# Kernel tuning notes

Hardware: AMD Instinct MI355X
Metric: run time of the kernel (lower is better)

## Reference

```python
import jax, jax.numpy as jnp
import numpy as np

B, N, D, C = 256, 256, 512, 1024
EPS = 1e-12  # F.normalize eps


def _l2norm(x):
    n = jnp.linalg.norm(x, axis=-1, keepdims=True)
    return x / jnp.maximum(n, EPS)


def setup_inputs() -> dict:
    key = jax.random.key(0)
    k1, k2, k3 = jax.random.split(key, 3)
    return {
        "image_tokens": jax.random.normal(k1, (B, N, D), dtype=jnp.float32),
        "text_features": jax.random.normal(k2, (C, D), dtype=jnp.float32),
        "log_tau": jnp.asarray(np.log(0.07), dtype=jnp.float32),
        "log_attn_tau": jnp.asarray(np.log(0.07), dtype=jnp.float32),
        "pid_labels": jax.random.randint(k3, (B,), 0, C),
    }


def reference(image_tokens, text_features, log_tau, log_attn_tau, pid_labels):
    toks = _l2norm(image_tokens.astype(jnp.float32))        # [B,N,D]
    txt = _l2norm(text_features.astype(jnp.float32))        # [C,D]
    sims = jnp.einsum('bnd,cd->bnc', toks, txt)             # [B,N,C]
    gt = pid_labels.astype(jnp.int32)
    # sims[arange(B), :, gt] -> [B,N]
    sims_gt = jnp.take_along_axis(sims, gt[:, None, None], axis=2)[..., 0]
    attn_tau = jnp.clip(jnp.exp(log_attn_tau), 0.01, 1.0)
    w = jax.nn.softmax(sims_gt / attn_tau, axis=1)          # [B,N]
    logits = jnp.einsum('bn,bnc->bc', w, sims)              # [B,C]
    tau = jnp.clip(jnp.exp(log_tau), 0.01, 1.0)
    logits = logits / tau
    # cross_entropy with label_smoothing=0.0, mean reduction
    logp = jax.nn.log_softmax(logits, axis=-1)
    nll = -jnp.take_along_axis(logp, gt[:, None], axis=1)[:, 0]
    return jnp.mean(nll)
```

## Files before the change

kernel.cpp:

```cpp
#include <hip/hip_runtime.h>
#include <math.h>

#define Bb 256
#define Nn 256
#define Dd 512
#define Cc 1024
#define KC 8
#define KD (Dd / KC)

__device__ __forceinline__ float waveReduceSum(float v) {
    #pragma unroll
    for (int off = 32; off > 0; off >>= 1)
        v += __shfl_xor(v, off, 64);
    return v;
}
__device__ __forceinline__ float waveReduceMax(float v) {
    #pragma unroll
    for (int off = 32; off > 0; off >>= 1)
        v = fmaxf(v, __shfl_xor(v, off, 64));
    return v;
}

__global__ void k_txtnorm(const float* __restrict__ txt, float* __restrict__ txt_n) {
    const int c = blockIdx.x;
    const int lane = threadIdx.x;
    const float* row = txt + (size_t)c * Dd + lane * 8;
    float4 a = *(const float4*)row;
    float4 b = *(const float4*)(row + 4);
    float ss = a.x*a.x + a.y*a.y + a.z*a.z + a.w*a.w
             + b.x*b.x + b.y*b.y + b.z*b.z + b.w*b.w;
    ss = waveReduceSum(ss);
    const float inv = 1.0f / fmaxf(sqrtf(ss), 1e-12f);
    float* out = txt_n + (size_t)c * Dd + lane * 8;
    a.x *= inv; a.y *= inv; a.z *= inv; a.w *= inv;
    b.x *= inv; b.y *= inv; b.z *= inv; b.w *= inv;
    *(float4*)out = a;
    *(float4*)(out + 4) = b;
}

__global__ void k_transpose(const float* __restrict__ txt_n, float* __restrict__ txt_t) {
    __shared__ float tile[32][33];
    const int c0 = blockIdx.x * 32;
    const int d0 = blockIdx.y * 32;
    const int tx = threadIdx.x & 31;
    const int ty = threadIdx.x >> 5;
    #pragma unroll
    for (int r = ty; r < 32; r += 8)
        tile[r][tx] = txt_n[(size_t)(c0 + r) * Dd + d0 + tx];
    __syncthreads();
    #pragma unroll
    for (int r = ty; r < 32; r += 8)
        txt_t[(size_t)(d0 + r) * Cc + c0 + tx] = tile[tx][r];
}

__global__ void __launch_bounds__(1024) k_attn_q(const float* __restrict__ toks,
                                                 const float* __restrict__ txt_n,
                                                 const int* __restrict__ pid,
                                                 const float* __restrict__ log_attn_tau,
                                                 float* __restrict__ q) {
    const int b = blockIdx.x;
    const int tid = threadIdx.x;
    const int wv = tid >> 6;
    const int lane = tid & 63;
    __shared__ float xg[Dd];
    __shared__ float qpart_s[16][Dd];
    __shared__ float ms[16], Ss[16];
    const int g = pid[b];
    if (tid < Dd) xg[tid] = txt_n[(size_t)g * Dd + tid];
    __syncthreads();
    float at = expf(log_attn_tau[0]);
    at = fminf(fmaxf(at, 0.01f), 1.0f);
    const float iat = 1.0f / at;

    const float4 xg0 = *(const float4*)&xg[lane * 8];
    const float4 xg1 = *(const float4*)&xg[lane * 8 + 4];

    float m = -INFINITY, S = 0.0f;
    float qa[8] = {0.f, 0.f, 0.f, 0.f, 0.f, 0.f, 0.f, 0.f};

    const float* base = toks + ((size_t)b * Nn + wv * 16) * Dd + lane * 8;
    float4 t0 = *(const float4*)base;
    float4 t1 = *(const float4*)(base + 4);
    #pragma unroll 4
    for (int r = 0; r < 16; ++r) {
        float4 n0, n1;
        if (r < 15) {
            const float* p = base + (size_t)(r + 1) * Dd;
            n0 = *(const float4*)p;
            n1 = *(const float4*)(p + 4);
        }
        float dot = t0.x*xg0.x + t0.y*xg0.y + t0.z*xg0.z + t0.w*xg0.w
                  + t1.x*xg1.x + t1.y*xg1.y + t1.z*xg1.z + t1.w*xg1.w;
        float ss  = t0.x*t0.x + t0.y*t0.y + t0.z*t0.z + t0.w*t0.w
                  + t1.x*t1.x + t1.y*t1.y + t1.z*t1.z + t1.w*t1.w;
        dot = waveReduceSum(dot);
        ss = waveReduceSum(ss);
        const float inv = 1.0f / fmaxf(sqrtf(ss), 1e-12f);
        const float s = dot * inv;
        if (s > m) {
            const float sc = expf((m - s) * iat);
            S = S * sc + 1.0f;
            qa[0] = qa[0]*sc + inv*t0.x; qa[1] = qa[1]*sc + inv*t0.y;
            qa[2] = qa[2]*sc + inv*t0.z; qa[3] = qa[3]*sc + inv*t0.w;
            qa[4] = qa[4]*sc + inv*t1.x; qa[5] = qa[5]*sc + inv*t1.y;
            qa[6] = qa[6]*sc + inv*t1.z; qa[7] = qa[7]*sc + inv*t1.w;
            m = s;
        } else {
            const float e = expf((s - m) * iat);
            S += e;
            const float w = e * inv;
            qa[0] = fmaf(w, t0.x, qa[0]); qa[1] = fmaf(w, t0.y, qa[1]);
            qa[2] = fmaf(w, t0.z, qa[2]); qa[3] = fmaf(w, t0.w, qa[3]);
            qa[4] = fmaf(w, t1.x, qa[4]); qa[5] = fmaf(w, t1.y, qa[5]);
            qa[6] = fmaf(w, t1.z, qa[6]); qa[7] = fmaf(w, t1.w, qa[7]);
        }
        t0 = n0; t1 = n1;
    }
    #pragma unroll
    for (int j = 0; j < 8; ++j) qpart_s[wv][lane * 8 + j] = qa[j];
    if (lane == 0) { ms[wv] = m; Ss[wv] = S; }
    __syncthreads();
    if (tid < Dd) {
        float M = -INFINITY;
        #pragma unroll
        for (int w = 0; w < 16; ++w) M = fmaxf(M, ms[w]);
        float Stot = 0.f, acc = 0.f;
        #pragma unroll
        for (int w = 0; w < 16; ++w) {
            const float sc = expf((ms[w] - M) * iat);
            Stot = fmaf(Ss[w], sc, Stot);
            acc = fmaf(qpart_s[w][tid], sc, acc);
        }
        q[(size_t)b * Dd + tid] = acc / Stot;
    }
}

__global__ void k_logits(const float* __restrict__ q, const float* __restrict__ txt_t,
                         float* __restrict__ part) {
    const int b0 = blockIdx.x * 4;
    const int kc = blockIdx.y;
    const int d0 = kc * KD;
    const int t = threadIdx.x;
    __shared__ float qs[4][KD];
    {
        const int j = t >> 6, d = t & 63;
        qs[j][d] = q[(size_t)(b0 + j) * Dd + d0 + d];
    }
    __syncthreads();
    const float4* xt = (const float4*)txt_t;
    float4 a0 = {0,0,0,0}, a1 = {0,0,0,0}, a2 = {0,0,0,0}, a3 = {0,0,0,0};
    #pragma unroll 4
    for (int d = 0; d < KD; d += 4) {
        const float4 q0 = *(const float4*)&qs[0][d];
        const float4 q1 = *(const float4*)&qs[1][d];
        const float4 q2 = *(const float4*)&qs[2][d];
        const float4 q3 = *(const float4*)&qs[3][d];
        const float4 x0 = xt[(size_t)(d0 + d + 0) * (Cc / 4) + t];
        const float4 x1 = xt[(size_t)(d0 + d + 1) * (Cc / 4) + t];
        const float4 x2 = xt[(size_t)(d0 + d + 2) * (Cc / 4) + t];
        const float4 x3 = xt[(size_t)(d0 + d + 3) * (Cc / 4) + t];
        a0.x = fmaf(q0.x,x0.x,a0.x); a0.y = fmaf(q0.x,x0.y,a0.y); a0.z = fmaf(q0.x,x0.z,a0.z); a0.w = fmaf(q0.x,x0.w,a0.w);
        a0.x = fmaf(q0.y,x1.x,a0.x); a0.y = fmaf(q0.y,x1.y,a0.y); a0.z = fmaf(q0.y,x1.z,a0.z); a0.w = fmaf(q0.y,x1.w,a0.w);
        a0.x = fmaf(q0.z,x2.x,a0.x); a0.y = fmaf(q0.z,x2.y,a0.y); a0.z = fmaf(q0.z,x2.z,a0.z); a0.w = fmaf(q0.z,x2.w,a0.w);
        a0.x = fmaf(q0.w,x3.x,a0.x); a0.y = fmaf(q0.w,x3.y,a0.y); a0.z = fmaf(q0.w,x3.z,a0.z); a0.w = fmaf(q0.w,x3.w,a0.w);
        a1.x = fmaf(q1.x,x0.x,a1.x); a1.y = fmaf(q1.x,x0.y,a1.y); a1.z = fmaf(q1.x,x0.z,a1.z); a1.w = fmaf(q1.x,x0.w,a1.w);
        a1.x = fmaf(q1.y,x1.x,a1.x); a1.y = fmaf(q1.y,x1.y,a1.y); a1.z = fmaf(q1.y,x1.z,a1.z); a1.w = fmaf(q1.y,x1.w,a1.w);
        a1.x = fmaf(q1.z,x2.x,a1.x); a1.y = fmaf(q1.z,x2.y,a1.y); a1.z = fmaf(q1.z,x2.z,a1.z); a1.w = fmaf(q1.z,x2.w,a1.w);
        a1.x = fmaf(q1.w,x3.x,a1.x); a1.y = fmaf(q1.w,x3.y,a1.y); a1.z = fmaf(q1.w,x3.z,a1.z); a1.w = fmaf(q1.w,x3.w,a1.w);
        a2.x = fmaf(q2.x,x0.x,a2.x); a2.y = fmaf(q2.x,x0.y,a2.y); a2.z = fmaf(q2.x,x0.z,a2.z); a2.w = fmaf(q2.x,x0.w,a2.w);
        a2.x = fmaf(q2.y,x1.x,a2.x); a2.y = fmaf(q2.y,x1.y,a2.y); a2.z = fmaf(q2.y,x1.z,a2.z); a2.w = fmaf(q2.y,x1.w,a2.w);
        a2.x = fmaf(q2.z,x2.x,a2.x); a2.y = fmaf(q2.z,x2.y,a2.y); a2.z = fmaf(q2.z,x2.z,a2.z); a2.w = fmaf(q2.z,x2.w,a2.w);
        a2.x = fmaf(q2.w,x3.x,a2.x); a2.y = fmaf(q2.w,x3.y,a2.y); a2.z = fmaf(q2.w,x3.z,a2.z); a2.w = fmaf(q2.w,x3.w,a2.w);
        a3.x = fmaf(q3.x,x0.x,a3.x); a3.y = fmaf(q3.x,x0.y,a3.y); a3.z = fmaf(q3.x,x0.z,a3.z); a3.w = fmaf(q3.x,x0.w,a3.w);
        a3.x = fmaf(q3.y,x1.x,a3.x); a3.y = fmaf(q3.y,x1.y,a3.y); a3.z = fmaf(q3.y,x1.z,a3.z); a3.w = fmaf(q3.y,x1.w,a3.w);
        a3.x = fmaf(q3.z,x2.x,a3.x); a3.y = fmaf(q3.z,x2.y,a3.y); a3.z = fmaf(q3.z,x2.z,a3.z); a3.w = fmaf(q3.z,x2.w,a3.w);
        a3.x = fmaf(q3.w,x3.x,a3.x); a3.y = fmaf(q3.w,x3.y,a3.y); a3.z = fmaf(q3.w,x3.z,a3.z); a3.w = fmaf(q3.w,x3.w,a3.w);
    }
    float* pb = part + ((size_t)kc * Bb + b0) * Cc;
    ((float4*)(pb + 0 * Cc))[t] = a0;
    ((float4*)(pb + 1 * Cc))[t] = a1;
    ((float4*)(pb + 2 * Cc))[t] = a2;
    ((float4*)(pb + 3 * Cc))[t] = a3;
}

__global__ void k_lse(const float* __restrict__ part, const int* __restrict__ pid,
                      const float* __restrict__ log_tau, float* __restrict__ nll) {
    const int b = blockIdx.x;
    const int t = threadIdx.x;
    float4 l = {0,0,0,0};
    #pragma unroll
    for (int kc = 0; kc < KC; ++kc) {
        const float4 p = ((const float4*)(part + ((size_t)kc * Bb + b) * Cc))[t];
        l.x += p.x; l.y += p.y; l.z += p.z; l.w += p.w;
    }
    float tau = expf(log_tau[0]);
    tau = fminf(fmaxf(tau, 0.01f), 1.0f);
    const float itau = 1.0f / tau;
    l.x *= itau; l.y *= itau; l.z *= itau; l.w *= itau;

    const int g = pid[b];
    __shared__ float redm[4], reds[4], sgt;
    if ((g >> 2) == t) {
        const float v[4] = {l.x, l.y, l.z, l.w};
        sgt = v[g & 3];
    }
    float m = fmaxf(fmaxf(l.x, l.y), fmaxf(l.z, l.w));
    m = waveReduceMax(m);
    if ((t & 63) == 0) redm[t >> 6] = m;
    __syncthreads();
    m = fmaxf(fmaxf(redm[0], redm[1]), fmaxf(redm[2], redm[3]));
    float e = expf(l.x - m) + expf(l.y - m) + expf(l.z - m) + expf(l.w - m);
    e = waveReduceSum(e);
    if ((t & 63) == 0) reds[t >> 6] = e;
    __syncthreads();
    if (t == 0) {
        const float S = reds[0] + reds[1] + reds[2] + reds[3];
        nll[b] = m + logf(S) - sgt;
    }
}

__global__ void k_mean(const float* __restrict__ nll, float* __restrict__ out) {
    float v = nll[threadIdx.x];
    __shared__ float red[4];
    v = waveReduceSum(v);
    if ((threadIdx.x & 63) == 0) red[threadIdx.x >> 6] = v;
    __syncthreads();
    if (threadIdx.x == 0) out[0] = (red[0] + red[1] + red[2] + red[3]) * (1.0f / (float)Bb);
}

extern "C" void kernel_launch(void* const* d_in, const int* in_sizes, int n_in,
                              void* d_out, int out_size, void* d_ws, size_t ws_size,
                              hipStream_t stream) {
    const float* toks = (const float*)d_in[0];
    const float* txt = (const float*)d_in[1];
    const float* log_tau = (const float*)d_in[2];
    const float* log_attn_tau = (const float*)d_in[3];
    const int* pid = (const int*)d_in[4];
    float* out = (float*)d_out;

    float* ws = (float*)d_ws;
    float* txt_n = ws;
    float* txt_t = txt_n + (size_t)Cc * Dd;
    float* q     = txt_t + (size_t)Dd * Cc;
    float* part  = q + (size_t)Bb * Dd;
    float* nll   = part + (size_t)KC * Bb * Cc;

    k_txtnorm<<<Cc, 64, 0, stream>>>(txt, txt_n);
    k_transpose<<<dim3(Cc / 32, Dd / 32), 256, 0, stream>>>(txt_n, txt_t);
    k_attn_q<<<Bb, 1024, 0, stream>>>(toks, txt_n, pid, log_attn_tau, q);
    k_logits<<<dim3(Bb / 4, KC), 256, 0, stream>>>(q, txt_t, part);
    k_lse<<<Bb, 256, 0, stream>>>(part, pid, log_tau, nll);
    k_mean<<<1, 256, 0, stream>>>(nll, out);
}
```

Before: 219.1 us.

## Fuse text normalization with transpose and fold mean into LSE via atomics

Merges the text-normalization and transpose kernels into one prep kernel that loads 16 rows into padded shared memory, computes per-row inverse norms, and writes the normalized transposed matrix directly. The separate normalized copy is dropped, and attention reads raw text scaled by the stored inverse norm. The final mean kernel is removed: each LSE block atomically adds its scaled NLL into an output zeroed by a memset. This cuts launches and one full pass over the text matrix, at the cost of nondeterministic float summation order and a memset call.

Measured after the change: 222.6 us. No clear change (+1.6%).

```diff
diff --git a/kernel.cpp b/kernel.cpp
--- a/kernel.cpp
+++ b/kernel.cpp
@@ -7,6 +7,8 @@
 #define Cc 1024
 #define KC 8
 #define KD (Dd / KC)
+#define PR 16
+#define PSTR 516
 
 __device__ __forceinline__ float waveReduceSum(float v) {
     #pragma unroll
@@ -21,40 +23,51 @@
     return v;
 }
 
-__global__ void k_txtnorm(const float* __restrict__ txt, float* __restrict__ txt_n) {
-    const int c = blockIdx.x;
-    const int lane = threadIdx.x;
-    const float* row = txt + (size_t)c * Dd + lane * 8;
-    float4 a = *(const float4*)row;
-    float4 b = *(const float4*)(row + 4);
-    float ss = a.x*a.x + a.y*a.y + a.z*a.z + a.w*a.w
-             + b.x*b.x + b.y*b.y + b.z*b.z + b.w*b.w;
-    ss = waveReduceSum(ss);
-    const float inv = 1.0f / fmaxf(sqrtf(ss), 1e-12f);
-    float* out = txt_n + (size_t)c * Dd + lane * 8;
-    a.x *= inv; a.y *= inv; a.z *= inv; a.w *= inv;
-    b.x *= inv; b.y *= inv; b.z *= inv; b.w *= inv;
-    *(float4*)out = a;
-    *(float4*)(out + 4) = b;
-}
-
-__global__ void k_transpose(const float* __restrict__ txt_n, float* __restrict__ txt_t) {
-    __shared__ float tile[32][33];
-    const int c0 = blockIdx.x * 32;
-    const int d0 = blockIdx.y * 32;
-    const int tx = threadIdx.x & 31;
-    const int ty = threadIdx.x >> 5;
-    #pragma unroll
-    for (int r = ty; r < 32; r += 8)
-        tile[r][tx] = txt_n[(size_t)(c0 + r) * Dd + d0 + tx];
-    __syncthreads();
-    #pragma unroll
-    for (int r = ty; r < 32; r += 8)
-        txt_t[(size_t)(d0 + r) * Cc + c0 + tx] = tile[tx][r];
+__global__ void k_prep(const float* __restrict__ txt, float* __restrict__ txt_t,
+                       float* __restrict__ invc) {
+    __shared__ float tile[PR * PSTR];
+    __shared__ float invs[PR];
+    const int c0 = blockIdx.x * PR;
+    const int tid = threadIdx.x;
+    #pragma unroll
+    for (int i = tid; i < PR * 128; i += 256) {
+        const int r = i >> 7, c4 = i & 127;
+        const float4 v = *(const float4*)(txt + (size_t)(c0 + r) * Dd + c4 * 4);
+        *(float4*)&tile[r * PSTR + c4 * 4] = v;
+    }
+    __syncthreads();
+    {
+        const int r = tid >> 4, k = tid & 15;
+        float s = 0.f;
+        #pragma unroll
+        for (int i = 0; i < 32; ++i) {
+            const float x = tile[r * PSTR + i * 16 + k];
+            s = fmaf(x, x, s);
+        }
+        s += __shfl_xor(s, 1, 64);
+        s += __shfl_xor(s, 2, 64);
+        s += __shfl_xor(s, 4, 64);
+        s += __shfl_xor(s, 8, 64);
+        if (k == 0) {
+            const float inv = 1.0f / fmaxf(sqrtf(s), 1e-12f);
+            invs[r] = inv;
+            invc[c0 + r] = inv;
+        }
+    }
+    __syncthreads();
+    {
+        const int c = tid & 15;
+        const int d0 = tid >> 4;
+        const float inv = invs[c];
+        #pragma unroll
+        for (int d = d0; d < Dd; d += 16)
+            txt_t[(size_t)d * Cc + c0 + c] = tile[c * PSTR + d] * inv;
+    }
 }
 
 __global__ void __launch_bounds__(1024) k_attn_q(const float* __restrict__ toks,
-                                                 const float* __restrict__ txt_n,
+                                                 const float* __restrict__ txt,
+                                                 const float* __restrict__ invc,
                                                  const int* __restrict__ pid,
                                                  const float* __restrict__ log_attn_tau,
                                                  float* __restrict__ q) {
@@ -66,7 +79,7 @@
     __shared__ float qpart_s[16][Dd];
     __shared__ float ms[16], Ss[16];
     const int g = pid[b];
-    if (tid < Dd) xg[tid] = txt_n[(size_t)g * Dd + tid];
+    if (tid < Dd) xg[tid] = txt[(size_t)g * Dd + tid] * invc[g];
     __syncthreads();
     float at = expf(log_attn_tau[0]);
     at = fminf(fmaxf(at, 0.01f), 1.0f);
@@ -184,7 +197,7 @@
 }
 
 __global__ void k_lse(const float* __restrict__ part, const int* __restrict__ pid,
-                      const float* __restrict__ log_tau, float* __restrict__ nll) {
+                      const float* __restrict__ log_tau, float* __restrict__ out) {
     const int b = blockIdx.x;
     const int t = threadIdx.x;
     float4 l = {0,0,0,0};
@@ -215,17 +228,9 @@
     __syncthreads();
     if (t == 0) {
         const float S = reds[0] + reds[1] + reds[2] + reds[3];
-        nll[b] = m + logf(S) - sgt;
-    }
-}
-
-__global__ void k_mean(const float* __restrict__ nll, float* __restrict__ out) {
-    float v = nll[threadIdx.x];
-    __shared__ float red[4];
-    v = waveReduceSum(v);
-    if ((threadIdx.x & 63) == 0) red[threadIdx.x >> 6] = v;
-    __syncthreads();
-    if (threadIdx.x == 0) out[0] = (red[0] + red[1] + red[2] + red[3]) * (1.0f / (float)Bb);
+        const float nll = m + logf(S) - sgt;
+        atomicAdd(out, nll * (1.0f / (float)Bb));
+    }
 }
 
 extern "C" void kernel_launch(void* const* d_in, const int* in_sizes, int n_in,
@@ -239,16 +244,14 @@
     float* out = (float*)d_out;
 
     float* ws = (float*)d_ws;
-    float* txt_n = ws;
-    float* txt_t = txt_n + (size_t)Cc * Dd;
-    float* q     = txt_t + (size_t)Dd * Cc;
+    float* txt_t = ws;
+    float* invc  = txt_t + (size_t)Dd * Cc;
+    float* q     = invc + Cc;
     float* part  = q + (size_t)Bb * Dd;
-    float* nll   = part + (size_t)KC * Bb * Cc;
-
-    k_txtnorm<<<Cc, 64, 0, stream>>>(txt, txt_n);
-    k_transpose<<<dim3(Cc / 32, Dd / 32), 256, 0, stream>>>(txt_n, txt_t);
-    k_attn_q<<<Bb, 1024, 0, stream>>>(toks, txt_n, pid, log_attn_tau, q);
+
+    hipMemsetAsync(out, 0, sizeof(float), stream);
+    k_prep<<<Cc / PR, 256, 0, stream>>>(txt, txt_t, invc);
+    k_attn_q<<<Bb, 1024, 0, stream>>>(toks, txt, invc, pid, log_attn_tau, q);
     k_logits<<<dim3(Bb / 4, KC), 256, 0, stream>>>(q, txt_t, part);
-    k_lse<<<Bb, 256, 0, stream>>>(part, pid, log_tau, nll);
-    k_mean<<<1, 256, 0, stream>>>(nll, out);
-}
+    k_lse<<<Bb, 256, 0, stream>>>(part, pid, log_tau, out);
+}
```
